# Optimization experiments

Measured on AMD Instinct MI355X. Metric: run time of the kernel, lower is better.

## Reference

```python
import jax, jax.numpy as jnp
import numpy as np

B, L, D, H = 64, 24, 512, 512


def setup_inputs() -> dict:
    key = jax.random.key(0)
    ks = jax.random.split(key, 6)
    inp = jax.random.normal(ks[0], (B, L, D), jnp.float32)
    length = jax.random.randint(ks[1], (B,), L // 2, L + 1)  # valid lengths in [L/2, L]
    # word_linear: word_dim -> 2*hidden_dim (kaiming normal, zero bias)
    word_W = jax.random.normal(ks[2], (2 * H, D), jnp.float32) * (2.0 / D) ** 0.5
    word_b = jnp.zeros((2 * H,), jnp.float32)
    # comp_linear: 2*hidden_dim -> 5*hidden_dim (TreeLSTM gates i, fl, fr, u, o)
    comp_W = jax.random.normal(ks[3], (5 * H, 2 * H), jnp.float32) * (1.0 / H) ** 0.5
    comp_b = jnp.zeros((5 * H,), jnp.float32)
    comp_query = jax.random.normal(ks[4], (H,), jnp.float32) * 0.01
    return dict(inp=inp, length=length, word_W=word_W, word_b=word_b,
                comp_W=comp_W, comp_b=comp_b, comp_query=comp_query)


def _tree_lstm_forward(inp, word_W, word_b, comp_W, comp_b, comp_query, length):
    max_depth = inp.shape[1]
    length_mask = jnp.arange(max_depth)[None, :] < length[:, None]  # (B, L) bool
    # leaf states: word_linear output chunked into (h, c)
    hc = inp @ word_W.T + word_b  # (B, L, 2H)
    h, c = jnp.split(hc, 2, axis=2)
    for i in range(max_depth - 1):  # sequential merge over shrinking length
        hl, cl = h[:, :-1, :], c[:, :-1, :]
        hr, cr = h[:, 1:, :], c[:, 1:, :]
        # BinaryTreeLSTMLayer: fused gate linear on [hl; hr]
        v = jnp.concatenate([hl, hr], axis=2) @ comp_W.T + comp_b  # (B, L-i-1, 5H)
        gi, gfl, gfr, gu, go = jnp.split(v, 5, axis=2)
        new_c = (cl * jax.nn.sigmoid(gfl + 1.0)
                 + cr * jax.nn.sigmoid(gfr + 1.0)
                 + jnp.tanh(gu) * jax.nn.sigmoid(gi))
        new_h = jax.nn.sigmoid(go) * jnp.tanh(new_c)
        if i < max_depth - 2:
            # select_composition: greedy (eval-mode) one-hot over query-dot scores
            scores = jnp.einsum('blh,h->bl', new_h, comp_query)  # (B, L-i-1)
            m = length_mask[:, i + 1:]
            masked = jnp.where(m, scores, -1e9)
            sel = jax.lax.stop_gradient(
                jax.nn.one_hot(jnp.argmax(masked, axis=1), masked.shape[1], dtype=new_h.dtype))
            cum = jnp.cumsum(sel, axis=1)
            left = 1.0 - cum
            right = jnp.concatenate(
                [jnp.zeros((sel.shape[0], 1), sel.dtype), cum[:, :-1]], axis=1)
            new_h = sel[..., None] * new_h + left[..., None] * hl + right[..., None] * hr
            new_c = sel[..., None] * new_c + left[..., None] * cl + right[..., None] * cr
        # update_state: only advance rows whose sequence is still active
        done = length_mask[:, i + 1].astype(new_h.dtype)[:, None, None]
        h = done * new_h + (1.0 - done) * h[:, :-1, :]
        c = done * new_c + (1.0 - done) * c[:, :-1, :]
    return h[:, 0, :]  # (B, H) root hidden state


def reference(inp, length, word_W, word_b, comp_W, comp_b, comp_query):
    return _tree_lstm_forward(inp, word_W, word_b, comp_W, comp_b, comp_query, length)
```

## Files before the change

### kernel.cpp

```cpp
#include <hip/hip_runtime.h>
#include <math.h>

#define BB 64
#define LL 24
#define DD 512
#define GG 2560
#define NSTEP 23
#define NTILES 160

__device__ __forceinline__ float sigm(float x) { return 1.0f / (1.0f + __expf(-x)); }

__device__ __forceinline__ unsigned short f2bf(float x) {
    unsigned u = __float_as_uint(x);
    unsigned r = (u + 0x7fff + ((u >> 16) & 1)) >> 16;
    return (unsigned short)r;
}
__device__ __forceinline__ float bf2f(unsigned short b) {
    return __uint_as_float(((unsigned)b) << 16);
}

using short8 = __attribute__((ext_vector_type(8))) short;
using f32x4 = __attribute__((ext_vector_type(4))) float;

__global__ __launch_bounds__(256) void splitW_k(const float* __restrict__ comp_W,
                                                unsigned short* __restrict__ Wh,
                                                unsigned short* __restrict__ Wl) {
    int t = (blockIdx.x * 256 + threadIdx.x) * 4;
    int n = t >> 9;
    int k = t & 511;
    const float* src = (n < GG) ? (comp_W + (size_t)n * (2 * DD) + k)
                                : (comp_W + (size_t)(n - GG) * (2 * DD) + DD + k);
    float4 v = *(const float4*)src;
    ushort4 h, l;
    h.x = f2bf(v.x); l.x = f2bf(v.x - bf2f(h.x));
    h.y = f2bf(v.y); l.y = f2bf(v.y - bf2f(h.y));
    h.z = f2bf(v.z); l.z = f2bf(v.z - bf2f(h.z));
    h.w = f2bf(v.w); l.w = f2bf(v.w - bf2f(h.w));
    *(ushort4*)(Wh + t) = h;
    *(ushort4*)(Wl + t) = l;
}

__global__ __launch_bounds__(256) void splitF_k(const float* __restrict__ src,
                                                unsigned short* __restrict__ dh,
                                                unsigned short* __restrict__ dl) {
    int t = (blockIdx.x * 256 + threadIdx.x) * 4;
    float4 v = *(const float4*)(src + t);
    ushort4 h, l;
    h.x = f2bf(v.x); l.x = f2bf(v.x - bf2f(h.x));
    h.y = f2bf(v.y); l.y = f2bf(v.y - bf2f(h.y));
    h.z = f2bf(v.z); l.z = f2bf(v.z - bf2f(h.z));
    h.w = f2bf(v.w); l.w = f2bf(v.w - bf2f(h.w));
    *(ushort4*)(dh + t) = h;
    *(ushort4*)(dl + t) = l;
}

__global__ __launch_bounds__(256) void gemm64w_mfma(
    const unsigned short* __restrict__ Ih, const unsigned short* __restrict__ Il,
    const unsigned short* __restrict__ Vh, const unsigned short* __restrict__ Vl,
    const float* __restrict__ bias,
    unsigned short* __restrict__ Ah, unsigned short* __restrict__ Al,
    float* __restrict__ O1) {
    __shared__ unsigned short AhS[64][72];
    __shared__ unsigned short AlS[64][72];
    __shared__ unsigned short BhS[128][72];
    __shared__ unsigned short BlS[128][72];

    const int tid = threadIdx.x;
    const int m0 = (blockIdx.x % 24) * 64;
    const int n0 = (blockIdx.x / 24) * 128;

    const int w = tid >> 6, lane = tid & 63;
    const int mq = w >> 1, nq = w & 1;
    const int lr = lane & 15, kg = lane >> 4;

    const int srow = tid >> 3;
    const int sk8 = tid & 7;

    const unsigned short* agh = Ih + (size_t)(m0 + srow) * DD + sk8 * 8;
    const unsigned short* agl = Il + (size_t)(m0 + srow) * DD + sk8 * 8;
    const unsigned short* bgh = Vh + (size_t)(n0 + srow) * DD + sk8 * 8;
    const unsigned short* bgl = Vl + (size_t)(n0 + srow) * DD + sk8 * 8;

    f32x4 acc[2][4];
#pragma unroll
    for (int mt = 0; mt < 2; ++mt)
#pragma unroll
        for (int nt = 0; nt < 4; ++nt) acc[mt][nt] = (f32x4){0.f, 0.f, 0.f, 0.f};

    short8 rAh[2], rAl[2], rBh[4], rBl[4];

#define LOADT(kt)                                                            \
    {                                                                        \
        _Pragma("unroll")                                                    \
        for (int it = 0; it < 2; ++it) {                                     \
            const size_t ro = (size_t)it * 32 * DD + (kt);                   \
            rAh[it] = *(const short8*)(agh + ro);                            \
            rAl[it] = *(const short8*)(agl + ro);                            \
        }                                                                    \
        _Pragma("unroll")                                                    \
        for (int it = 0; it < 4; ++it) {                                     \
            const size_t ro = (size_t)it * 32 * DD + (kt);                   \
            rBh[it] = *(const short8*)(bgh + ro);                            \
            rBl[it] = *(const short8*)(bgl + ro);                            \
        }                                                                    \
    }
#define WRITET()                                                             \
    {                                                                        \
        _Pragma("unroll")                                                    \
        for (int it = 0; it < 2; ++it) {                                     \
            const int row = srow + it * 32;                                  \
            *(short8*)&AhS[row][sk8 * 8] = rAh[it];                          \
            *(short8*)&AlS[row][sk8 * 8] = rAl[it];                          \
        }                                                                    \
        _Pragma("unroll")                                                    \
        for (int it = 0; it < 4; ++it) {                                     \
            const int row = srow + it * 32;                                  \
            *(short8*)&BhS[row][sk8 * 8] = rBh[it];                          \
            *(short8*)&BlS[row][sk8 * 8] = rBl[it];                          \
        }                                                                    \
    }

    LOADT(0);
    WRITET();
    __syncthreads();

    for (int kti = 0; kti < 8; ++kti) {
        if (kti + 1 < 8) LOADT((kti + 1) * 64);
#pragma unroll
        for (int ks2 = 0; ks2 < 2; ++ks2) {
            const int kb = ks2 * 32 + kg * 8;
            short8 fah[2], fal[2], fbh[4], fbl[4];
#pragma unroll
            for (int t = 0; t < 2; ++t) {
                fah[t] = *(const short8*)&AhS[mq * 32 + t * 16 + lr][kb];
                fal[t] = *(const short8*)&AlS[mq * 32 + t * 16 + lr][kb];
            }
#pragma unroll
            for (int t = 0; t < 4; ++t) {
                fbh[t] = *(const short8*)&BhS[nq * 64 + t * 16 + lr][kb];
                fbl[t] = *(const short8*)&BlS[nq * 64 + t * 16 + lr][kb];
            }
#pragma unroll
            for (int mt = 0; mt < 2; ++mt)
#pragma unroll
                for (int nt = 0; nt < 4; ++nt) {
                    acc[mt][nt] = __builtin_amdgcn_mfma_f32_16x16x32_bf16(fal[mt], fbh[nt], acc[mt][nt], 0, 0, 0);
                    acc[mt][nt] = __builtin_amdgcn_mfma_f32_16x16x32_bf16(fah[mt], fbl[nt], acc[mt][nt], 0, 0, 0);
                    acc[mt][nt] = __builtin_amdgcn_mfma_f32_16x16x32_bf16(fah[mt], fbh[nt], acc[mt][nt], 0, 0, 0);
                }
        }
        __syncthreads();
        if (kti + 1 < 8) {
            WRITET();
            __syncthreads();
        }
    }
#undef LOADT
#undef WRITET

#pragma unroll
    for (int mt = 0; mt < 2; ++mt) {
        const int mbase = m0 + mq * 32 + mt * 16 + kg * 4;
#pragma unroll
        for (int nt = 0; nt < 4; ++nt) {
            const int n = n0 + nq * 64 + nt * 16 + lr;
            const float bv = bias[n];
#pragma unroll
            for (int r = 0; r < 4; ++r) {
                const int m = mbase + r;
                float v = acc[mt][nt][r] + bv;
                if (n < DD) {
                    unsigned short hv = f2bf(v);
                    Ah[(size_t)m * DD + n] = hv;
                    Al[(size_t)m * DD + n] = f2bf(v - bf2f(hv));
                } else {
                    O1[(size_t)m * DD + (n - DD)] = v;
                }
            }
        }
    }
}

__global__ __launch_bounds__(256) void gemm_big_mfma(
    const unsigned short* __restrict__ Ah, const unsigned short* __restrict__ Al,
    const unsigned short* __restrict__ Wh, const unsigned short* __restrict__ Wl,
    float* __restrict__ O0, float* __restrict__ O1) {
    __shared__ unsigned short AhS[128][72];
    __shared__ unsigned short AlS[128][72];
    __shared__ unsigned short BhS[128][72];
    __shared__ unsigned short BlS[128][72];

    const int tid = threadIdx.x;
    const int xcd = blockIdx.x & 7, idx = blockIdx.x >> 3;
    const int n0 = (xcd * 5 + idx % 5) * 128;
    const int m0 = (idx / 5) * 128;

    const int w = tid >> 6, lane = tid & 63;
    const int mq = w >> 1, nq = w & 1;
    const int lr = lane & 15, kg = lane >> 4;

    const int srow = tid >> 3;
    const int sk8 = tid & 7;

    const unsigned short* agh = Ah + (size_t)(m0 + srow) * DD + sk8 * 8;
    const unsigned short* agl = Al + (size_t)(m0 + srow) * DD + sk8 * 8;
    const unsigned short* bgh = Wh + (size_t)(n0 + srow) * DD + sk8 * 8;
    const unsigned short* bgl = Wl + (size_t)(n0 + srow) * DD + sk8 * 8;

    f32x4 acc[4][4];
#pragma unroll
    for (int mt = 0; mt < 4; ++mt)
#pragma unroll
        for (int nt = 0; nt < 4; ++nt) acc[mt][nt] = (f32x4){0.f, 0.f, 0.f, 0.f};

    short8 rAh[4], rAl[4], rBh[4], rBl[4];

#define LOADT(kt)                                                            \
    {                                                                        \
        _Pragma("unroll")                                                    \
        for (int it = 0; it < 4; ++it) {                                     \
            const size_t ro = (size_t)it * 32 * DD + (kt);                   \
            rAh[it] = *(const short8*)(agh + ro);                            \
            rAl[it] = *(const short8*)(agl + ro);                            \
            rBh[it] = *(const short8*)(bgh + ro);                            \
            rBl[it] = *(const short8*)(bgl + ro);                            \
        }                                                                    \
    }
#define WRITET()                                                             \
    {                                                                        \
        _Pragma("unroll")                                                    \
        for (int it = 0; it < 4; ++it) {                                     \
            const int row = srow + it * 32;                                  \
            *(short8*)&AhS[row][sk8 * 8] = rAh[it];                          \
            *(short8*)&AlS[row][sk8 * 8] = rAl[it];                          \
            *(short8*)&BhS[row][sk8 * 8] = rBh[it];                          \
            *(short8*)&BlS[row][sk8 * 8] = rBl[it];                          \
        }                                                                    \
    }

    LOADT(0);
    WRITET();
    __syncthreads();

    for (int kti = 0; kti < 8; ++kti) {
        if (kti + 1 < 8) LOADT((kti + 1) * 64);
#pragma unroll
        for (int ks2 = 0; ks2 < 2; ++ks2) {
            const int kb = ks2 * 32 + kg * 8;
            short8 fah[4], fal[4], fbh[4], fbl[4];
#pragma unroll
            for (int t = 0; t < 4; ++t) {
                fah[t] = *(const short8*)&AhS[mq * 64 + t * 16 + lr][kb];
                fal[t] = *(const short8*)&AlS[mq * 64 + t * 16 + lr][kb];
                fbh[t] = *(const short8*)&BhS[nq * 64 + t * 16 + lr][kb];
                fbl[t] = *(const short8*)&BlS[nq * 64 + t * 16 + lr][kb];
            }
#pragma unroll
            for (int mt = 0; mt < 4; ++mt)
#pragma unroll
                for (int nt = 0; nt < 4; ++nt) {
                    acc[mt][nt] = __builtin_amdgcn_mfma_f32_16x16x32_bf16(fal[mt], fbh[nt], acc[mt][nt], 0, 0, 0);
                    acc[mt][nt] = __builtin_amdgcn_mfma_f32_16x16x32_bf16(fah[mt], fbl[nt], acc[mt][nt], 0, 0, 0);
                    acc[mt][nt] = __builtin_amdgcn_mfma_f32_16x16x32_bf16(fah[mt], fbh[nt], acc[mt][nt], 0, 0, 0);
                }
        }
        __syncthreads();
        if (kti + 1 < 8) {
            WRITET();
            __syncthreads();
        }
    }
#undef LOADT
#undef WRITET

#pragma unroll
    for (int mt = 0; mt < 4; ++mt) {
        const int mbase = m0 + mq * 64 + mt * 16 + kg * 4;
#pragma unroll
        for (int nt = 0; nt < 4; ++nt) {
            const int n = n0 + nq * 64 + nt * 16 + lr;
#pragma unroll
            for (int r = 0; r < 4; ++r) {
                const int m = mbase + r;
                float* dst = (n < GG) ? (O0 + (size_t)m * GG + n)
                                      : (O1 + (size_t)m * GG + (n - GG));
                *dst = acc[mt][nt][r];
            }
        }
    }
}

__device__ __forceinline__ float half_dot(const float* __restrict__ ar,
                                          const float* __restrict__ br,
                                          const float* __restrict__ cb,
                                          const float* __restrict__ cl,
                                          const float* __restrict__ cr,
                                          const float* __restrict__ q, int lane) {
    float part = 0.f;
#pragma unroll
    for (int d = lane; d < DD; d += 128) {
        float gi = ar[d] + br[d] + cb[d];
        float gfl = ar[DD + d] + br[DD + d] + cb[DD + d];
        float gfr = ar[2 * DD + d] + br[2 * DD + d] + cb[2 * DD + d];
        float gu = ar[3 * DD + d] + br[3 * DD + d] + cb[3 * DD + d];
        float go = ar[4 * DD + d] + br[4 * DD + d] + cb[4 * DD + d];
        float nc = cl[d] * sigm(gfl + 1.f) + cr[d] * sigm(gfr + 1.f) + tanhf(gu) * sigm(gi);
        part += sigm(go) * tanhf(nc) * q[d];
    }
#pragma unroll
    for (int off = 32; off; off >>= 1) part += __shfl_down(part, off);
    return part;
}

__device__ __forceinline__ void gate2n(const float* __restrict__ ar,
                                       const float* __restrict__ br,
                                       const float* __restrict__ cb,
                                       const float* __restrict__ cl,
                                       const float* __restrict__ cr, int d,
                                       float nh[2], float nc[2]) {
    float2 A0 = *(const float2*)(ar + d),          B0 = *(const float2*)(br + d);
    float2 A1 = *(const float2*)(ar + DD + d),     B1 = *(const float2*)(br + DD + d);
    float2 A2 = *(const float2*)(ar + 2 * DD + d), B2 = *(const float2*)(br + 2 * DD + d);
    float2 A3 = *(const float2*)(ar + 3 * DD + d), B3 = *(const float2*)(br + 3 * DD + d);
    float2 A4 = *(const float2*)(ar + 4 * DD + d), B4 = *(const float2*)(br + 4 * DD + d);
    float2 C0 = *(const float2*)(cb + d);
    float2 C1 = *(const float2*)(cb + DD + d);
    float2 C2 = *(const float2*)(cb + 2 * DD + d);
    float2 C3 = *(const float2*)(cb + 3 * DD + d);
    float2 C4 = *(const float2*)(cb + 4 * DD + d);
    float2 CL = *(const float2*)(cl + d);
    float2 CR = *(const float2*)(cr + d);
    float gi0 = A0.x + B0.x + C0.x, gi1 = A0.y + B0.y + C0.y;
    float gfl0 = A1.x + B1.x + C1.x, gfl1 = A1.y + B1.y + C1.y;
    float gfr0 = A2.x + B2.x + C2.x, gfr1 = A2.y + B2.y + C2.y;
    float gu0 = A3.x + B3.x + C3.x, gu1 = A3.y + B3.y + C3.y;
    float go0 = A4.x + B4.x + C4.x, go1 = A4.y + B4.y + C4.y;
    nc[0] = CL.x * sigm(gfl0 + 1.f) + CR.x * sigm(gfr0 + 1.f) + tanhf(gu0) * sigm(gi0);
    nc[1] = CL.y * sigm(gfl1 + 1.f) + CR.y * sigm(gfr1 + 1.f) + tanhf(gu1) * sigm(gi1);
    nh[0] = sigm(go0) * tanhf(nc[0]);
    nh[1] = sigm(go1) * tanhf(nc[1]);
}

__global__ __launch_bounds__(256) void scoreall_k(const float* __restrict__ acache,
                                                  const float* __restrict__ bcache,
                                                  const float* __restrict__ cbuf,
                                                  const float* __restrict__ compb,
                                                  const float* __restrict__ q,
                                                  float* __restrict__ scores_g) {
    __shared__ float red_s[4];
    const int tid = threadIdx.x;
    const int b = blockIdx.y;
    const int p = blockIdx.x * 2 + (tid >> 7);
    const bool valid = p < NSTEP;
    float w = 0.f;
    if (valid) {
        w = half_dot(acache + (size_t)(b * LL + p) * GG,
                     bcache + (size_t)(b * LL + p + 1) * GG, compb,
                     cbuf + (size_t)(b * LL + p) * DD,
                     cbuf + (size_t)(b * LL + p + 1) * DD, q, tid & 127);
    }
    if ((tid & 63) == 0) red_s[tid >> 6] = w;
    __syncthreads();
    if ((tid == 0 || tid == 128) && valid) {
        int base = tid >> 6;
        scores_g[b * NSTEP + p] = red_s[base] + red_s[base + 1];
    }
}

__global__ __launch_bounds__(256) void stepA_k(
    int i, const int* __restrict__ length, float* __restrict__ cbuf,
    const float* __restrict__ acache, const float* __restrict__ bcache,
    float* __restrict__ hout, unsigned short* __restrict__ hh,
    unsigned short* __restrict__ hl, float* __restrict__ scores_g,
    int* __restrict__ seq_g, int* __restrict__ kp_g, int* __restrict__ msel,
    const float* __restrict__ compb, const float* __restrict__ q, float* __restrict__ out) {
    __shared__ float red_s[4];
    __shared__ float sc_l[32];
    __shared__ int seq_l[32];
    __shared__ int k_sh;
    const int tid = threadIdx.x;
    const int b = blockIdx.x;
    const int lane7 = tid & 127;
    const int lenb = length[b];
    const int ncand = NSTEP - i;

    if (i == 0) {
        if (tid < LL) seq_l[tid] = tid;
    } else {
        if (tid < LL - i) seq_l[tid] = seq_g[b * 32 + tid];
    }
    if (tid < ncand) sc_l[tid] = scores_g[b * NSTEP + tid];
    __syncthreads();
    const int kp = (i > 0) ? kp_g[b] : 0;

    if (i > 0 && i < lenb) {
        int p = (tid < 128) ? (kp - 1) : kp;
        bool valid = (p >= 0) && (p < ncand);
        float w = 0.f;
        if (valid) {
            int sl = seq_l[p], sr = seq_l[p + 1];
            const float* ar = acache + (size_t)(b * LL + sl) * GG;
            const float* br = bcache + (size_t)(b * LL + sr) * GG;
            const float* cl = cbuf + (size_t)(b * LL + sl) * DD;
            const float* cr = cbuf + (size_t)(b * LL + sr) * DD;
#pragma unroll
            for (int pass = 0; pass < 2; ++pass) {
                int d = pass * 256 + lane7 * 2;
                float nh[2], nc[2];
                gate2n(ar, br, compb, cl, cr, d, nh, nc);
                float2 Q = *(const float2*)(q + d);
                w += nh[0] * Q.x + nh[1] * Q.y;
            }
#pragma unroll
            for (int off = 32; off; off >>= 1) w += __shfl_down(w, off);
        }
        if ((tid & 63) == 0) red_s[tid >> 6] = w;
        __syncthreads();
        if (tid == 0) {
            if (kp - 1 >= 0) sc_l[kp - 1] = red_s[0] + red_s[1];
            if (kp < ncand) sc_l[kp] = red_s[2] + red_s[3];
        }
        __syncthreads();
    }

    if (i + 1 < lenb) {
        if (tid == 0) {
            const int vmax = lenb - i - 2;
            int k = 0;
            float best = sc_l[0];
            for (int pp = 1; pp <= vmax; ++pp)
                if (sc_l[pp] > best) { best = sc_l[pp]; k = pp; }
            k_sh = k;
        }
        __syncthreads();
        const int k = k_sh;
        const int sl = seq_l[k], sr = seq_l[k + 1];
        const float* ar = acache + (size_t)(b * LL + sl) * GG;
        const float* br = bcache + (size_t)(b * LL + sr) * GG;
        const float* cl = cbuf + (size_t)(b * LL + sl) * DD;
        const float* cr = cbuf + (size_t)(b * LL + sr) * DD;
        {
            const int d = 2 * tid;
            float nh[2], nc[2];
            gate2n(ar, br, compb, cl, cr, d, nh, nc);
            *(float2*)(cbuf + (size_t)(b * LL + sl) * DD + d) = make_float2(nc[0], nc[1]);
            *(float2*)(hout + (size_t)b * DD + d) = make_float2(nh[0], nh[1]);
            ushort2 hv, lv;
            hv.x = f2bf(nh[0]); lv.x = f2bf(nh[0] - bf2f(hv.x));
            hv.y = f2bf(nh[1]); lv.y = f2bf(nh[1] - bf2f(hv.y));
            *(ushort2*)(hh + (size_t)b * DD + d) = hv;
            *(ushort2*)(hl + (size_t)b * DD + d) = lv;
            if (i == NSTEP - 1)
                *(float2*)(out + (size_t)b * DD + d) = make_float2(nh[0], nh[1]);
        }
        float sv = (tid + 1 < ncand) ? sc_l[tid + 1] : 0.f;
        int qv = (tid + 1 < LL - i) ? seq_l[tid + 1] : 0;
        __syncthreads();
        if (tid >= k + 1 && tid <= ncand - 2) sc_l[tid] = sv;
        if (tid >= k + 1 && tid <= LL - i - 2) seq_l[tid] = qv;
        if (tid < ncand - 1) scores_g[b * NSTEP + tid] = sc_l[tid];
        if (tid < LL - i - 1) seq_g[b * 32 + tid] = seq_l[tid];
        if (tid == 0) { kp_g[b] = k; msel[b] = sl; }
    } else if (i == NSTEP - 1) {
        const int d = 2 * tid;
        *(float2*)(out + (size_t)b * DD + d) = *(const float2*)(hout + (size_t)b * DD + d);
    }
}

__global__ __launch_bounds__(256) void stepB_mfma(
    const unsigned short* __restrict__ hh, const unsigned short* __restrict__ hl,
    const int* __restrict__ msel,
    const unsigned short* __restrict__ Wh, const unsigned short* __restrict__ Wl,
    float* __restrict__ acache, float* __restrict__ bcache) {
    __shared__ int msel_s[BB];
    const int tid = threadIdx.x;
    const int bid = blockIdx.x;
    if (tid < BB) msel_s[tid] = msel[tid];
    __syncthreads();

    const int w = tid >> 6, lane = tid & 63;
    const int mt0 = (w >> 1) * 2;
    const int nt = w & 1;
    const int lr = lane & 15;
    const int kg = lane >> 4;
    const int n = bid * 32 + nt * 16 + lr;

    const unsigned short* wh_row = Wh + (size_t)n * DD;
    const unsigned short* wl_row = Wl + (size_t)n * DD;
    const unsigned short* a0h_row = hh + (size_t)(mt0 * 16 + lr) * DD;
    const unsigned short* a0l_row = hl + (size_t)(mt0 * 16 + lr) * DD;
    const unsigned short* a1h_row = a0h_row + 16 * DD;
    const unsigned short* a1l_row = a0l_row + 16 * DD;

    f32x4 acc0 = {0.f, 0.f, 0.f, 0.f};
    f32x4 acc1 = {0.f, 0.f, 0.f, 0.f};

#pragma unroll 4
    for (int ks = 0; ks < 16; ++ks) {
        const int kb = ks * 32 + kg * 8;
        short8 bh = *(const short8*)(wh_row + kb);
        short8 bl = *(const short8*)(wl_row + kb);
        short8 a0h = *(const short8*)(a0h_row + kb);
        short8 a0l = *(const short8*)(a0l_row + kb);
        short8 a1h = *(const short8*)(a1h_row + kb);
        short8 a1l = *(const short8*)(a1l_row + kb);
        acc0 = __builtin_amdgcn_mfma_f32_16x16x32_bf16(a0h, bh, acc0, 0, 0, 0);
        acc1 = __builtin_amdgcn_mfma_f32_16x16x32_bf16(a1h, bh, acc1, 0, 0, 0);
        acc0 = __builtin_amdgcn_mfma_f32_16x16x32_bf16(a0l, bh, acc0, 0, 0, 0);
        acc1 = __builtin_amdgcn_mfma_f32_16x16x32_bf16(a1l, bh, acc1, 0, 0, 0);
        acc0 = __builtin_amdgcn_mfma_f32_16x16x32_bf16(a0h, bl, acc0, 0, 0, 0);
        acc1 = __builtin_amdgcn_mfma_f32_16x16x32_bf16(a1h, bl, acc1, 0, 0, 0);
    }

#pragma unroll
    for (int t = 0; t < 2; ++t) {
        f32x4 acc = t ? acc1 : acc0;
        const int mbase = (mt0 + t) * 16 + kg * 4;
#pragma unroll
        for (int r = 0; r < 4; ++r) {
            int m = mbase + r;
            size_t row = (size_t)(m * LL + msel_s[m]);
            float* dst = (n < GG) ? (acache + row * GG + n)
                                  : (bcache + row * GG + (n - GG));
            *dst = acc[r];
        }
    }
}

extern "C" void kernel_launch(void* const* d_in, const int* in_sizes, int n_in, void* d_out,
                              int out_size, void* d_ws, size_t ws_size, hipStream_t stream) {
    const float* inp = (const float*)d_in[0];
    const int* length = (const int*)d_in[1];
    const float* word_W = (const float*)d_in[2];
    const float* word_b = (const float*)d_in[3];
    const float* comp_W = (const float*)d_in[4];
    const float* comp_b = (const float*)d_in[5];
    const float* comp_q = (const float*)d_in[6];
    float* out = (float*)d_out;

    float* ws = (float*)d_ws;
    size_t off = 0;
    float* cbuf = ws + off;   off += (size_t)BB * LL * DD;
    float* acache = ws + off; off += (size_t)BB * LL * GG;
    float* bcache = ws + off; off += (size_t)BB * LL * GG;
    float* hout = ws + off;   off += (size_t)BB * DD;
    float* scores = ws + off; off += 2048;
    int* seq_g = (int*)(ws + off); off += BB * 32;
    int* kp_g = (int*)(ws + off);  off += 64;
    int* msel = (int*)(ws + off);  off += 64;
    unsigned short* Wh = (unsigned short*)(ws + off); off += (size_t)5120 * DD / 2;
    unsigned short* Wl = (unsigned short*)(ws + off); off += (size_t)5120 * DD / 2;
    unsigned short* hh = (unsigned short*)(ws + off); off += (size_t)BB * DD / 2;
    unsigned short* hl = (unsigned short*)(ws + off); off += (size_t)BB * DD / 2;
    unsigned short* Ah = (unsigned short*)(ws + off); off += (size_t)BB * LL * DD / 2;
    unsigned short* Al = (unsigned short*)(ws + off); off += (size_t)BB * LL * DD / 2;
    unsigned short* Ih = (unsigned short*)(ws + off); off += (size_t)BB * LL * DD / 2;
    unsigned short* Il = (unsigned short*)(ws + off); off += (size_t)BB * LL * DD / 2;
    unsigned short* Vh = (unsigned short*)(ws + off); off += (size_t)1024 * DD / 2;
    unsigned short* Vl = (unsigned short*)(ws + off); off += (size_t)1024 * DD / 2;
    (void)ws_size; (void)in_sizes; (void)n_in; (void)out_size;

    splitW_k<<<2560, 256, 0, stream>>>(comp_W, Wh, Wl);
    splitF_k<<<768, 256, 0, stream>>>(inp, Ih, Il);
    splitF_k<<<512, 256, 0, stream>>>(word_W, Vh, Vl);

    gemm64w_mfma<<<192, 256, 0, stream>>>(Ih, Il, Vh, Vl, word_b, Ah, Al, cbuf);

    gemm_big_mfma<<<480, 256, 0, stream>>>(Ah, Al, Wh, Wl, acache, bcache);

    scoreall_k<<<dim3(12, 64), 256, 0, stream>>>(acache, bcache, cbuf, comp_b, comp_q, scores);

    for (int i = 0; i < NSTEP; ++i) {
        stepA_k<<<BB, 256, 0, stream>>>(i, length, cbuf, acache, bcache, hout, hh, hl,
                                        scores, seq_g, kp_g, msel, comp_b, comp_q, out);
        if (i < NSTEP - 1) {
            stepB_mfma<<<NTILES, 256, 0, stream>>>(hh, hl, msel, Wh, Wl, acache, bcache);
        }
    }
}
```

Measured before the change: 585.2 us.

## Interleave gate columns and fuse neighbor rescoring into stepB GEMM epilogue

The comp_W rows and bias are permuted so the five gates for each pair of hidden units sit next to each other, letting each stepB block own complete gate groups. The re-scoring of the two candidates next to the merged node moves out of the serial stepA kernel and into the stepB epilogue. There it runs on freshly computed gate values kept in shared memory and is accumulated into scores with atomics, while stepA zeroes those slots beforehand. This shortens the latency-bound per-step stepA work at the cost of more complex stepB tiles (128 blocks with padded 48-wide N tiles) and atomic accumulation order.

```diff
diff --git a/kernel.cpp b/kernel.cpp
--- a/kernel.cpp
+++ b/kernel.cpp
@@ -6,7 +6,8 @@
 #define DD 512
 #define GG 2560
 #define NSTEP 23
-#define NTILES 160
+#define NBB 128
+
 
 __device__ __forceinline__ float sigm(float x) { return 1.0f / (1.0f + __expf(-x)); }
 
@@ -21,6 +22,26 @@
 
 using short8 = __attribute__((ext_vector_type(8))) short;
 using f32x4 = __attribute__((ext_vector_type(4))) float;
+
+__device__ __forceinline__ void gatepair(const float* ar, const float* br,
+                                         const float* cb,
+                                         float cl0, float cl1, float cr0, float cr1,
+                                         float nh[2], float nc[2]) {
+    float2 A0 = *(const float2*)(ar + 0), B0 = *(const float2*)(br + 0), C0 = *(const float2*)(cb + 0);
+    float2 A1 = *(const float2*)(ar + 2), B1 = *(const float2*)(br + 2), C1 = *(const float2*)(cb + 2);
+    float2 A2 = *(const float2*)(ar + 4), B2 = *(const float2*)(br + 4), C2 = *(const float2*)(cb + 4);
+    float2 A3 = *(const float2*)(ar + 6), B3 = *(const float2*)(br + 6), C3 = *(const float2*)(cb + 6);
+    float2 A4 = *(const float2*)(ar + 8), B4 = *(const float2*)(br + 8), C4 = *(const float2*)(cb + 8);
+    float gi0 = A0.x + B0.x + C0.x, gi1 = A0.y + B0.y + C0.y;
+    float gfl0 = A1.x + B1.x + C1.x, gfl1 = A1.y + B1.y + C1.y;
+    float gfr0 = A2.x + B2.x + C2.x, gfr1 = A2.y + B2.y + C2.y;
+    float gu0 = A3.x + B3.x + C3.x, gu1 = A3.y + B3.y + C3.y;
+    float go0 = A4.x + B4.x + C4.x, go1 = A4.y + B4.y + C4.y;
+    nc[0] = cl0 * sigm(gfl0 + 1.f) + cr0 * sigm(gfr0 + 1.f) + tanhf(gu0) * sigm(gi0);
+    nc[1] = cl1 * sigm(gfl1 + 1.f) + cr1 * sigm(gfr1 + 1.f) + tanhf(gu1) * sigm(gi1);
+    nh[0] = sigm(go0) * tanhf(nc[0]);
+    nh[1] = sigm(go1) * tanhf(nc[1]);
+}
 
 __global__ __launch_bounds__(256) void splitW_k(const float* __restrict__ comp_W,
                                                 unsigned short* __restrict__ Wh,
@@ -28,8 +49,11 @@
     int t = (blockIdx.x * 256 + threadIdx.x) * 4;
     int n = t >> 9;
     int k = t & 511;
-    const float* src = (n < GG) ? (comp_W + (size_t)n * (2 * DD) + k)
-                                : (comp_W + (size_t)(n - GG) * (2 * DD) + DD + k);
+    int p = (n >= GG) ? 1 : 0;
+    int r = n - p * GG;
+    int g = (r % 10) >> 1;
+    int d = (r / 10) * 2 + (r & 1);
+    const float* src = comp_W + (size_t)(g * 512 + d) * (2 * DD) + p * DD + k;
     float4 v = *(const float4*)src;
     ushort4 h, l;
     h.x = f2bf(v.x); l.x = f2bf(v.x - bf2f(h.x));
@@ -38,6 +62,14 @@
     h.w = f2bf(v.w); l.w = f2bf(v.w - bf2f(h.w));
     *(ushort4*)(Wh + t) = h;
     *(ushort4*)(Wl + t) = l;
+}
+
+__global__ __launch_bounds__(256) void compbp_k(const float* __restrict__ comp_b,
+                                                float* __restrict__ cbp) {
+    int c = blockIdx.x * 256 + threadIdx.x;
+    int g = (c % 10) >> 1;
+    int d = (c / 10) * 2 + (c & 1);
+    cbp[c] = comp_b[g * 512 + d];
 }
 
 __global__ __launch_bounds__(256) void splitF_k(const float* __restrict__ src,
@@ -292,59 +324,29 @@
 
 __device__ __forceinline__ float half_dot(const float* __restrict__ ar,
                                           const float* __restrict__ br,
-                                          const float* __restrict__ cb,
+                                          const float* __restrict__ cbp,
                                           const float* __restrict__ cl,
                                           const float* __restrict__ cr,
                                           const float* __restrict__ q, int lane) {
     float part = 0.f;
 #pragma unroll
-    for (int d = lane; d < DD; d += 128) {
-        float gi = ar[d] + br[d] + cb[d];
-        float gfl = ar[DD + d] + br[DD + d] + cb[DD + d];
-        float gfr = ar[2 * DD + d] + br[2 * DD + d] + cb[2 * DD + d];
-        float gu = ar[3 * DD + d] + br[3 * DD + d] + cb[3 * DD + d];
-        float go = ar[4 * DD + d] + br[4 * DD + d] + cb[4 * DD + d];
-        float nc = cl[d] * sigm(gfl + 1.f) + cr[d] * sigm(gfr + 1.f) + tanhf(gu) * sigm(gi);
-        part += sigm(go) * tanhf(nc) * q[d];
+    for (int pr = lane; pr < 256; pr += 128) {
+        const int base = pr * 10, d0 = pr * 2;
+        float nh[2], nc[2];
+        gatepair(ar + base, br + base, cbp + base,
+                 cl[d0], cl[d0 + 1], cr[d0], cr[d0 + 1], nh, nc);
+        float2 Q = *(const float2*)(q + d0);
+        part += nh[0] * Q.x + nh[1] * Q.y;
     }
 #pragma unroll
     for (int off = 32; off; off >>= 1) part += __shfl_down(part, off);
     return part;
-}
-
-__device__ __forceinline__ void gate2n(const float* __restrict__ ar,
-                                       const float* __restrict__ br,
-                                       const float* __restrict__ cb,
-                                       const float* __restrict__ cl,
-                                       const float* __restrict__ cr, int d,
-                                       float nh[2], float nc[2]) {
-    float2 A0 = *(const float2*)(ar + d),          B0 = *(const float2*)(br + d);
-    float2 A1 = *(const float2*)(ar + DD + d),     B1 = *(const float2*)(br + DD + d);
-    float2 A2 = *(const float2*)(ar + 2 * DD + d), B2 = *(const float2*)(br + 2 * DD + d);
-    float2 A3 = *(const float2*)(ar + 3 * DD + d), B3 = *(const float2*)(br + 3 * DD + d);
-    float2 A4 = *(const float2*)(ar + 4 * DD + d), B4 = *(const float2*)(br + 4 * DD + d);
-    float2 C0 = *(const float2*)(cb + d);
-    float2 C1 = *(const float2*)(cb + DD + d);
-    float2 C2 = *(const float2*)(cb + 2 * DD + d);
-    float2 C3 = *(const float2*)(cb + 3 * DD + d);
-    float2 C4 = *(const float2*)(cb + 4 * DD + d);
-    float2 CL = *(const float2*)(cl + d);
-    float2 CR = *(const float2*)(cr + d);
-    float gi0 = A0.x + B0.x + C0.x, gi1 = A0.y + B0.y + C0.y;
-    float gfl0 = A1.x + B1.x + C1.x, gfl1 = A1.y + B1.y + C1.y;
-    float gfr0 = A2.x + B2.x + C2.x, gfr1 = A2.y + B2.y + C2.y;
-    float gu0 = A3.x + B3.x + C3.x, gu1 = A3.y + B3.y + C3.y;
-    float go0 = A4.x + B4.x + C4.x, go1 = A4.y + B4.y + C4.y;
-    nc[0] = CL.x * sigm(gfl0 + 1.f) + CR.x * sigm(gfr0 + 1.f) + tanhf(gu0) * sigm(gi0);
-    nc[1] = CL.y * sigm(gfl1 + 1.f) + CR.y * sigm(gfr1 + 1.f) + tanhf(gu1) * sigm(gi1);
-    nh[0] = sigm(go0) * tanhf(nc[0]);
-    nh[1] = sigm(go1) * tanhf(nc[1]);
 }
 
 __global__ __launch_bounds__(256) void scoreall_k(const float* __restrict__ acache,
                                                   const float* __restrict__ bcache,
                                                   const float* __restrict__ cbuf,
-                                                  const float* __restrict__ compb,
+                                                  const float* __restrict__ cbp,
                                                   const float* __restrict__ q,
                                                   float* __restrict__ scores_g) {
     __shared__ float red_s[4];
@@ -355,7 +357,7 @@
     float w = 0.f;
     if (valid) {
         w = half_dot(acache + (size_t)(b * LL + p) * GG,
-                     bcache + (size_t)(b * LL + p + 1) * GG, compb,
+                     bcache + (size_t)(b * LL + p + 1) * GG, cbp,
                      cbuf + (size_t)(b * LL + p) * DD,
                      cbuf + (size_t)(b * LL + p + 1) * DD, q, tid & 127);
     }
@@ -372,15 +374,14 @@
     const float* __restrict__ acache, const float* __restrict__ bcache,
     float* __restrict__ hout, unsigned short* __restrict__ hh,
     unsigned short* __restrict__ hl, float* __restrict__ scores_g,
-    int* __restrict__ seq_g, int* __restrict__ kp_g, int* __restrict__ msel,
-    const float* __restrict__ compb, const float* __restrict__ q, float* __restrict__ out) {
-    __shared__ float red_s[4];
+    int* __restrict__ seq_g, int4* __restrict__ rescInfo, int* __restrict__ msel,
+    const float* __restrict__ cbp, const float* __restrict__ q,
+    float* __restrict__ out) {
     __shared__ float sc_l[32];
     __shared__ int seq_l[32];
     __shared__ int k_sh;
     const int tid = threadIdx.x;
     const int b = blockIdx.x;
-    const int lane7 = tid & 127;
     const int lenb = length[b];
     const int ncand = NSTEP - i;
 
@@ -391,37 +392,6 @@
     }
     if (tid < ncand) sc_l[tid] = scores_g[b * NSTEP + tid];
     __syncthreads();
-    const int kp = (i > 0) ? kp_g[b] : 0;
-
-    if (i > 0 && i < lenb) {
-        int p = (tid < 128) ? (kp - 1) : kp;
-        bool valid = (p >= 0) && (p < ncand);
-        float w = 0.f;
-        if (valid) {
-            int sl = seq_l[p], sr = seq_l[p + 1];
-            const float* ar = acache + (size_t)(b * LL + sl) * GG;
-            const float* br = bcache + (size_t)(b * LL + sr) * GG;
-            const float* cl = cbuf + (size_t)(b * LL + sl) * DD;
-            const float* cr = cbuf + (size_t)(b * LL + sr) * DD;
-#pragma unroll
-            for (int pass = 0; pass < 2; ++pass) {
-                int d = pass * 256 + lane7 * 2;
-                float nh[2], nc[2];
-                gate2n(ar, br, compb, cl, cr, d, nh, nc);
-                float2 Q = *(const float2*)(q + d);
-                w += nh[0] * Q.x + nh[1] * Q.y;
-            }
-#pragma unroll
-            for (int off = 32; off; off >>= 1) w += __shfl_down(w, off);
-        }
-        if ((tid & 63) == 0) red_s[tid >> 6] = w;
-        __syncthreads();
-        if (tid == 0) {
-            if (kp - 1 >= 0) sc_l[kp - 1] = red_s[0] + red_s[1];
-            if (kp < ncand) sc_l[kp] = red_s[2] + red_s[3];
-        }
-        __syncthreads();
-    }
 
     if (i + 1 < lenb) {
         if (tid == 0) {
@@ -435,14 +405,20 @@
         __syncthreads();
         const int k = k_sh;
         const int sl = seq_l[k], sr = seq_l[k + 1];
+        int sLn = 0, sRn = 0;
+        if (tid == 0) {
+            sLn = (k > 0) ? seq_l[k - 1] : 0;
+            sRn = (k < ncand - 1) ? seq_l[k + 2] : 0;
+        }
         const float* ar = acache + (size_t)(b * LL + sl) * GG;
         const float* br = bcache + (size_t)(b * LL + sr) * GG;
         const float* cl = cbuf + (size_t)(b * LL + sl) * DD;
         const float* cr = cbuf + (size_t)(b * LL + sr) * DD;
         {
-            const int d = 2 * tid;
+            const int d = 2 * tid, base = tid * 10;
             float nh[2], nc[2];
-            gate2n(ar, br, compb, cl, cr, d, nh, nc);
+            gatepair(ar + base, br + base, cbp + base,
+                     cl[d], cl[d + 1], cr[d], cr[d + 1], nh, nc);
             *(float2*)(cbuf + (size_t)(b * LL + sl) * DD + d) = make_float2(nc[0], nc[1]);
             *(float2*)(hout + (size_t)b * DD + d) = make_float2(nh[0], nh[1]);
             ushort2 hv, lv;
@@ -458,71 +434,130 @@
         __syncthreads();
         if (tid >= k + 1 && tid <= ncand - 2) sc_l[tid] = sv;
         if (tid >= k + 1 && tid <= LL - i - 2) seq_l[tid] = qv;
-        if (tid < ncand - 1) scores_g[b * NSTEP + tid] = sc_l[tid];
+        if (tid < ncand - 1)
+            scores_g[b * NSTEP + tid] = (tid == k - 1 || tid == k) ? 0.f : sc_l[tid];
         if (tid < LL - i - 1) seq_g[b * 32 + tid] = seq_l[tid];
-        if (tid == 0) { kp_g[b] = k; msel[b] = sl; }
-    } else if (i == NSTEP - 1) {
-        const int d = 2 * tid;
-        *(float2*)(out + (size_t)b * DD + d) = *(const float2*)(hout + (size_t)b * DD + d);
+        if (tid == 0) {
+            msel[b] = sl;
+            int fl = ((k > 0) ? 1 : 0) | ((k < ncand - 1) ? 2 : 0);
+            rescInfo[b] = make_int4(k, sLn, sRn, fl);
+        }
+    } else {
+        if (tid == 0) rescInfo[b] = make_int4(0, 0, 0, 0);
+        if (i == NSTEP - 1) {
+            const int d = 2 * tid;
+            *(float2*)(out + (size_t)b * DD + d) = *(const float2*)(hout + (size_t)b * DD + d);
+        }
     }
 }
 
 __global__ __launch_bounds__(256) void stepB_mfma(
     const unsigned short* __restrict__ hh, const unsigned short* __restrict__ hl,
-    const int* __restrict__ msel,
+    const int* __restrict__ msel, const int4* __restrict__ rescInfo,
     const unsigned short* __restrict__ Wh, const unsigned short* __restrict__ Wl,
-    float* __restrict__ acache, float* __restrict__ bcache) {
+    const float* __restrict__ cbuf, const float* __restrict__ cbp,
+    const float* __restrict__ q,
+    float* __restrict__ acache, float* __restrict__ bcache,
+    float* __restrict__ scores_g) {
+    __shared__ float newv[64][44];
     __shared__ int msel_s[BB];
+    __shared__ int4 ri_s[BB];
     const int tid = threadIdx.x;
-    const int bid = blockIdx.x;
-    if (tid < BB) msel_s[tid] = msel[tid];
+    const int j = blockIdx.x;
+    if (tid < BB) { msel_s[tid] = msel[tid]; ri_s[tid] = rescInfo[tid]; }
     __syncthreads();
 
     const int w = tid >> 6, lane = tid & 63;
-    const int mt0 = (w >> 1) * 2;
-    const int nt = w & 1;
-    const int lr = lane & 15;
-    const int kg = lane >> 4;
-    const int n = bid * 32 + nt * 16 + lr;
-
-    const unsigned short* wh_row = Wh + (size_t)n * DD;
-    const unsigned short* wl_row = Wl + (size_t)n * DD;
-    const unsigned short* a0h_row = hh + (size_t)(mt0 * 16 + lr) * DD;
-    const unsigned short* a0l_row = hl + (size_t)(mt0 * 16 + lr) * DD;
-    const unsigned short* a1h_row = a0h_row + 16 * DD;
-    const unsigned short* a1l_row = a0l_row + 16 * DD;
+    const int lr = lane & 15, kg = lane >> 4;
+
+    int wr[3];
+#pragma unroll
+    for (int nt = 0; nt < 3; ++nt) {
+        int t = nt * 16 + lr;
+        wr[nt] = (t < 20) ? (j * 20 + t) : ((t < 40) ? (GG + j * 20 + (t - 20)) : 0);
+    }
+    const unsigned short* b0h = Wh + (size_t)wr[0] * DD;
+    const unsigned short* b0l = Wl + (size_t)wr[0] * DD;
+    const unsigned short* b1h = Wh + (size_t)wr[1] * DD;
+    const unsigned short* b1l = Wl + (size_t)wr[1] * DD;
+    const unsigned short* b2h = Wh + (size_t)wr[2] * DD;
+    const unsigned short* b2l = Wl + (size_t)wr[2] * DD;
+    const unsigned short* arow_h = hh + (size_t)(w * 16 + lr) * DD;
+    const unsigned short* arow_l = hl + (size_t)(w * 16 + lr) * DD;
 
     f32x4 acc0 = {0.f, 0.f, 0.f, 0.f};
     f32x4 acc1 = {0.f, 0.f, 0.f, 0.f};
+    f32x4 acc2 = {0.f, 0.f, 0.f, 0.f};
 
 #pragma unroll 4
     for (int ks = 0; ks < 16; ++ks) {
         const int kb = ks * 32 + kg * 8;
-        short8 bh = *(const short8*)(wh_row + kb);
-        short8 bl = *(const short8*)(wl_row + kb);
-        short8 a0h = *(const short8*)(a0h_row + kb);
-        short8 a0l = *(const short8*)(a0l_row + kb);
-        short8 a1h = *(const short8*)(a1h_row + kb);
-        short8 a1l = *(const short8*)(a1l_row + kb);
-        acc0 = __builtin_amdgcn_mfma_f32_16x16x32_bf16(a0h, bh, acc0, 0, 0, 0);
-        acc1 = __builtin_amdgcn_mfma_f32_16x16x32_bf16(a1h, bh, acc1, 0, 0, 0);
-        acc0 = __builtin_amdgcn_mfma_f32_16x16x32_bf16(a0l, bh, acc0, 0, 0, 0);
-        acc1 = __builtin_amdgcn_mfma_f32_16x16x32_bf16(a1l, bh, acc1, 0, 0, 0);
-        acc0 = __builtin_amdgcn_mfma_f32_16x16x32_bf16(a0h, bl, acc0, 0, 0, 0);
-        acc1 = __builtin_amdgcn_mfma_f32_16x16x32_bf16(a1h, bl, acc1, 0, 0, 0);
-    }
-
-#pragma unroll
-    for (int t = 0; t < 2; ++t) {
-        f32x4 acc = t ? acc1 : acc0;
-        const int mbase = (mt0 + t) * 16 + kg * 4;
-#pragma unroll
-        for (int r = 0; r < 4; ++r) {
-            int m = mbase + r;
-            size_t row = (size_t)(m * LL + msel_s[m]);
-            float* dst = (n < GG) ? (acache + row * GG + n)
-                                  : (bcache + row * GG + (n - GG));
-            *dst = acc[r];
+        short8 ah = *(const short8*)(arow_h + kb);
+        short8 al = *(const short8*)(arow_l + kb);
+        short8 w0h = *(const short8*)(b0h + kb), w0l = *(const short8*)(b0l + kb);
+        short8 w1h = *(const short8*)(b1h + kb), w1l = *(const short8*)(b1l + kb);
+        short8 w2h = *(const short8*)(b2h + kb), w2l = *(const short8*)(b2l + kb);
+        acc0 = __builtin_amdgcn_mfma_f32_16x16x32_bf16(al, w0h, acc0, 0, 0, 0);
+        acc1 = __builtin_amdgcn_mfma_f32_16x16x32_bf16(al, w1h, acc1, 0, 0, 0);
+        acc2 = __builtin_amdgcn_mfma_f32_16x16x32_bf16(al, w2h, acc2, 0, 0, 0);
+        acc0 = __builtin_amdgcn_mfma_f32_16x16x32_bf16(ah, w0l, acc0, 0, 0, 0);
+        acc1 = __builtin_amdgcn_mfma_f32_16x16x32_bf16(ah, w1l, acc1, 0, 0, 0);
+        acc2 = __builtin_amdgcn_mfma_f32_16x16x32_bf16(ah, w2l, acc2, 0, 0, 0);
+        acc0 = __builtin_amdgcn_mfma_f32_16x16x32_bf16(ah, w0h, acc0, 0, 0, 0);
+        acc1 = __builtin_amdgcn_mfma_f32_16x16x32_bf16(ah, w1h, acc1, 0, 0, 0);
+        acc2 = __builtin_amdgcn_mfma_f32_16x16x32_bf16(ah, w2h, acc2, 0, 0, 0);
+    }
+
+#pragma unroll
+    for (int nt = 0; nt < 3; ++nt) {
+        f32x4 a = (nt == 0) ? acc0 : (nt == 1) ? acc1 : acc2;
+        const int t = nt * 16 + lr;
+        if (t < 40) {
+#pragma unroll
+            for (int r = 0; r < 4; ++r) {
+                const int bb = w * 16 + kg * 4 + r;
+                newv[bb][t] = a[r];
+                size_t row = (size_t)(bb * LL + msel_s[bb]);
+                float* dst = (t < 20) ? (acache + row * GG + j * 20 + t)
+                                      : (bcache + row * GG + j * 20 + (t - 20));
+                *dst = a[r];
+            }
+        }
+    }
+    __syncthreads();
+
+    if (tid < 128) {
+        const int bb = tid >> 1, pp = tid & 1;
+        const int4 ri = ri_s[bb];
+        const int k = ri.x, sL = ri.y, sR = ri.z, fl = ri.w;
+        const int sN = msel_s[bb];
+        const int gbase = j * 20 + pp * 10;
+        const int d0 = (2 * j + pp) * 2;
+        float2 Q = *(const float2*)(q + d0);
+        float s0 = 0.f, s1 = 0.f;
+        if (fl & 1) {
+            const float* arow = acache + (size_t)(bb * LL + sL) * GG + gbase;
+            const float* clp = cbuf + (size_t)(bb * LL + sL) * DD;
+            const float* crp = cbuf + (size_t)(bb * LL + sN) * DD;
+            float nh[2], nc[2];
+            gatepair(arow, &newv[bb][20 + pp * 10], cbp + gbase,
+                     clp[d0], clp[d0 + 1], crp[d0], crp[d0 + 1], nh, nc);
+            s0 = nh[0] * Q.x + nh[1] * Q.y;
+        }
+        if (fl & 2) {
+            const float* brow = bcache + (size_t)(bb * LL + sR) * GG + gbase;
+            const float* clp = cbuf + (size_t)(bb * LL + sN) * DD;
+            const float* crp = cbuf + (size_t)(bb * LL + sR) * DD;
+            float nh[2], nc[2];
+            gatepair(&newv[bb][pp * 10], brow, cbp + gbase,
+                     clp[d0], clp[d0 + 1], crp[d0], crp[d0 + 1], nh, nc);
+            s1 = nh[0] * Q.x + nh[1] * Q.y;
+        }
+        s0 += __shfl_xor(s0, 1);
+        s1 += __shfl_xor(s1, 1);
+        if (pp == 0) {
+            if (fl & 1) atomicAdd(scores_g + bb * NSTEP + (k - 1), s0);
+            if (fl & 2) atomicAdd(scores_g + bb * NSTEP + k, s1);
         }
     }
 }
@@ -546,8 +581,9 @@
     float* hout = ws + off;   off += (size_t)BB * DD;
     float* scores = ws + off; off += 2048;
     int* seq_g = (int*)(ws + off); off += BB * 32;
-    int* kp_g = (int*)(ws + off);  off += 64;
+    int4* rescInfo = (int4*)(ws + off); off += BB * 4;
     int* msel = (int*)(ws + off);  off += 64;
+    float* cbp = ws + off;    off += GG;
     unsigned short* Wh = (unsigned short*)(ws + off); off += (size_t)5120 * DD / 2;
     unsigned short* Wl = (unsigned short*)(ws + off); off += (size_t)5120 * DD / 2;
     unsigned short* hh = (unsigned short*)(ws + off); off += (size_t)BB * DD / 2;
@@ -561,6 +597,7 @@
     (void)ws_size; (void)in_sizes; (void)n_in; (void)out_size;
 
     splitW_k<<<2560, 256, 0, stream>>>(comp_W, Wh, Wl);
+    compbp_k<<<10, 256, 0, stream>>>(comp_b, cbp);
     splitF_k<<<768, 256, 0, stream>>>(inp, Ih, Il);
     splitF_k<<<512, 256, 0, stream>>>(word_W, Vh, Vl);
 
@@ -568,13 +605,15 @@
 
     gemm_big_mfma<<<480, 256, 0, stream>>>(Ah, Al, Wh, Wl, acache, bcache);
 
-    scoreall_k<<<dim3(12, 64), 256, 0, stream>>>(acache, bcache, cbuf, comp_b, comp_q, scores);
+    scoreall_k<<<dim3(12, 64), 256, 0, stream>>>(acache, bcache, cbuf, cbp, comp_q, scores);
 
     for (int i = 0; i < NSTEP; ++i) {
         stepA_k<<<BB, 256, 0, stream>>>(i, length, cbuf, acache, bcache, hout, hh, hl,
-                                        scores, seq_g, kp_g, msel, comp_b, comp_q, out);
+                                        scores, seq_g, rescInfo, msel, cbp, comp_q, out);
         if (i < NSTEP - 1) {
-            stepB_mfma<<<NTILES, 256, 0, stream>>>(hh, hl, msel, Wh, Wl, acache, bcache);
-        }
-    }
-}
+            stepB_mfma<<<NBB, 256, 0, stream>>>(hh, hl, msel, rescInfo, Wh, Wl,
+                                                cbuf, cbp, comp_q,
+                                                acache, bcache, scores);
+        }
+    }
+}
```

Result: slower. 721.5 us (+23.3%).

## Interleave gate rows of comp_W so each thread reads contiguous gate pairs

Applied to the files above, without the earlier changes.

The comp_W rows, and with them the acache/bcache gate columns and the bias, are permuted so that the five gates for each pair of hidden units sit in ten contiguous floats. The gate elementwise code then reads one contiguous 40-byte block per pair instead of five strided float2 loads spread 2KB apart. A small kernel builds the permuted bias. The cost is per-thread accesses that are less coalesced across lanes, since the lane stride becomes 40 bytes.

```diff
diff --git a/kernel.cpp b/kernel.cpp
--- a/kernel.cpp
+++ b/kernel.cpp
@@ -8,6 +8,7 @@
 #define NSTEP 23
 #define NTILES 160
 
+
 __device__ __forceinline__ float sigm(float x) { return 1.0f / (1.0f + __expf(-x)); }
 
 __device__ __forceinline__ unsigned short f2bf(float x) {
@@ -21,6 +22,26 @@
 
 using short8 = __attribute__((ext_vector_type(8))) short;
 using f32x4 = __attribute__((ext_vector_type(4))) float;
+
+__device__ __forceinline__ void gatepair(const float* ar, const float* br,
+                                         const float* cb,
+                                         float cl0, float cl1, float cr0, float cr1,
+                                         float nh[2], float nc[2]) {
+    float2 A0 = *(const float2*)(ar + 0), B0 = *(const float2*)(br + 0), C0 = *(const float2*)(cb + 0);
+    float2 A1 = *(const float2*)(ar + 2), B1 = *(const float2*)(br + 2), C1 = *(const float2*)(cb + 2);
+    float2 A2 = *(const float2*)(ar + 4), B2 = *(const float2*)(br + 4), C2 = *(const float2*)(cb + 4);
+    float2 A3 = *(const float2*)(ar + 6), B3 = *(const float2*)(br + 6), C3 = *(const float2*)(cb + 6);
+    float2 A4 = *(const float2*)(ar + 8), B4 = *(const float2*)(br + 8), C4 = *(const float2*)(cb + 8);
+    float gi0 = A0.x + B0.x + C0.x, gi1 = A0.y + B0.y + C0.y;
+    float gfl0 = A1.x + B1.x + C1.x, gfl1 = A1.y + B1.y + C1.y;
+    float gfr0 = A2.x + B2.x + C2.x, gfr1 = A2.y + B2.y + C2.y;
+    float gu0 = A3.x + B3.x + C3.x, gu1 = A3.y + B3.y + C3.y;
+    float go0 = A4.x + B4.x + C4.x, go1 = A4.y + B4.y + C4.y;
+    nc[0] = cl0 * sigm(gfl0 + 1.f) + cr0 * sigm(gfr0 + 1.f) + tanhf(gu0) * sigm(gi0);
+    nc[1] = cl1 * sigm(gfl1 + 1.f) + cr1 * sigm(gfr1 + 1.f) + tanhf(gu1) * sigm(gi1);
+    nh[0] = sigm(go0) * tanhf(nc[0]);
+    nh[1] = sigm(go1) * tanhf(nc[1]);
+}
 
 __global__ __launch_bounds__(256) void splitW_k(const float* __restrict__ comp_W,
                                                 unsigned short* __restrict__ Wh,
@@ -28,8 +49,11 @@
     int t = (blockIdx.x * 256 + threadIdx.x) * 4;
     int n = t >> 9;
     int k = t & 511;
-    const float* src = (n < GG) ? (comp_W + (size_t)n * (2 * DD) + k)
-                                : (comp_W + (size_t)(n - GG) * (2 * DD) + DD + k);
+    int p = (n >= GG) ? 1 : 0;
+    int r = n - p * GG;
+    int g = (r % 10) >> 1;
+    int d = (r / 10) * 2 + (r & 1);
+    const float* src = comp_W + (size_t)(g * 512 + d) * (2 * DD) + p * DD + k;
     float4 v = *(const float4*)src;
     ushort4 h, l;
     h.x = f2bf(v.x); l.x = f2bf(v.x - bf2f(h.x));
@@ -38,6 +62,14 @@
     h.w = f2bf(v.w); l.w = f2bf(v.w - bf2f(h.w));
     *(ushort4*)(Wh + t) = h;
     *(ushort4*)(Wl + t) = l;
+}
+
+__global__ __launch_bounds__(256) void compbp_k(const float* __restrict__ comp_b,
+                                                float* __restrict__ cbp) {
+    int c = blockIdx.x * 256 + threadIdx.x;
+    int g = (c % 10) >> 1;
+    int d = (c / 10) * 2 + (c & 1);
+    cbp[c] = comp_b[g * 512 + d];
 }
 
 __global__ __launch_bounds__(256) void splitF_k(const float* __restrict__ src,
@@ -292,59 +324,29 @@
 
 __device__ __forceinline__ float half_dot(const float* __restrict__ ar,
                                           const float* __restrict__ br,
-                                          const float* __restrict__ cb,
+                                          const float* __restrict__ cbp,
                                           const float* __restrict__ cl,
                                           const float* __restrict__ cr,
                                           const float* __restrict__ q, int lane) {
     float part = 0.f;
 #pragma unroll
-    for (int d = lane; d < DD; d += 128) {
-        float gi = ar[d] + br[d] + cb[d];
-        float gfl = ar[DD + d] + br[DD + d] + cb[DD + d];
-        float gfr = ar[2 * DD + d] + br[2 * DD + d] + cb[2 * DD + d];
-        float gu = ar[3 * DD + d] + br[3 * DD + d] + cb[3 * DD + d];
-        float go = ar[4 * DD + d] + br[4 * DD + d] + cb[4 * DD + d];
-        float nc = cl[d] * sigm(gfl + 1.f) + cr[d] * sigm(gfr + 1.f) + tanhf(gu) * sigm(gi);
-        part += sigm(go) * tanhf(nc) * q[d];
+    for (int pr = lane; pr < 256; pr += 128) {
+        const int base = pr * 10, d0 = pr * 2;
+        float nh[2], nc[2];
+        gatepair(ar + base, br + base, cbp + base,
+                 cl[d0], cl[d0 + 1], cr[d0], cr[d0 + 1], nh, nc);
+        float2 Q = *(const float2*)(q + d0);
+        part += nh[0] * Q.x + nh[1] * Q.y;
     }
 #pragma unroll
     for (int off = 32; off; off >>= 1) part += __shfl_down(part, off);
     return part;
-}
-
-__device__ __forceinline__ void gate2n(const float* __restrict__ ar,
-                                       const float* __restrict__ br,
-                                       const float* __restrict__ cb,
-                                       const float* __restrict__ cl,
-                                       const float* __restrict__ cr, int d,
-                                       float nh[2], float nc[2]) {
-    float2 A0 = *(const float2*)(ar + d),          B0 = *(const float2*)(br + d);
-    float2 A1 = *(const float2*)(ar + DD + d),     B1 = *(const float2*)(br + DD + d);
-    float2 A2 = *(const float2*)(ar + 2 * DD + d), B2 = *(const float2*)(br + 2 * DD + d);
-    float2 A3 = *(const float2*)(ar + 3 * DD + d), B3 = *(const float2*)(br + 3 * DD + d);
-    float2 A4 = *(const float2*)(ar + 4 * DD + d), B4 = *(const float2*)(br + 4 * DD + d);
-    float2 C0 = *(const float2*)(cb + d);
-    float2 C1 = *(const float2*)(cb + DD + d);
-    float2 C2 = *(const float2*)(cb + 2 * DD + d);
-    float2 C3 = *(const float2*)(cb + 3 * DD + d);
-    float2 C4 = *(const float2*)(cb + 4 * DD + d);
-    float2 CL = *(const float2*)(cl + d);
-    float2 CR = *(const float2*)(cr + d);
-    float gi0 = A0.x + B0.x + C0.x, gi1 = A0.y + B0.y + C0.y;
-    float gfl0 = A1.x + B1.x + C1.x, gfl1 = A1.y + B1.y + C1.y;
-    float gfr0 = A2.x + B2.x + C2.x, gfr1 = A2.y + B2.y + C2.y;
-    float gu0 = A3.x + B3.x + C3.x, gu1 = A3.y + B3.y + C3.y;
-    float go0 = A4.x + B4.x + C4.x, go1 = A4.y + B4.y + C4.y;
-    nc[0] = CL.x * sigm(gfl0 + 1.f) + CR.x * sigm(gfr0 + 1.f) + tanhf(gu0) * sigm(gi0);
-    nc[1] = CL.y * sigm(gfl1 + 1.f) + CR.y * sigm(gfr1 + 1.f) + tanhf(gu1) * sigm(gi1);
-    nh[0] = sigm(go0) * tanhf(nc[0]);
-    nh[1] = sigm(go1) * tanhf(nc[1]);
 }
 
 __global__ __launch_bounds__(256) void scoreall_k(const float* __restrict__ acache,
                                                   const float* __restrict__ bcache,
                                                   const float* __restrict__ cbuf,
-                                                  const float* __restrict__ compb,
+                                                  const float* __restrict__ cbp,
                                                   const float* __restrict__ q,
                                                   float* __restrict__ scores_g) {
     __shared__ float red_s[4];
@@ -355,7 +357,7 @@
     float w = 0.f;
     if (valid) {
         w = half_dot(acache + (size_t)(b * LL + p) * GG,
-                     bcache + (size_t)(b * LL + p + 1) * GG, compb,
+                     bcache + (size_t)(b * LL + p + 1) * GG, cbp,
                      cbuf + (size_t)(b * LL + p) * DD,
                      cbuf + (size_t)(b * LL + p + 1) * DD, q, tid & 127);
     }
@@ -373,14 +375,14 @@
     float* __restrict__ hout, unsigned short* __restrict__ hh,
     unsigned short* __restrict__ hl, float* __restrict__ scores_g,
     int* __restrict__ seq_g, int* __restrict__ kp_g, int* __restrict__ msel,
-    const float* __restrict__ compb, const float* __restrict__ q, float* __restrict__ out) {
+    const float* __restrict__ cbp, const float* __restrict__ q,
+    float* __restrict__ out) {
     __shared__ float red_s[4];
     __shared__ float sc_l[32];
     __shared__ int seq_l[32];
     __shared__ int k_sh;
     const int tid = threadIdx.x;
     const int b = blockIdx.x;
-    const int lane7 = tid & 127;
     const int lenb = length[b];
     const int ncand = NSTEP - i;
 
@@ -399,20 +401,10 @@
         float w = 0.f;
         if (valid) {
             int sl = seq_l[p], sr = seq_l[p + 1];
-            const float* ar = acache + (size_t)(b * LL + sl) * GG;
-            const float* br = bcache + (size_t)(b * LL + sr) * GG;
-            const float* cl = cbuf + (size_t)(b * LL + sl) * DD;
-            const float* cr = cbuf + (size_t)(b * LL + sr) * DD;
-#pragma unroll
-            for (int pass = 0; pass < 2; ++pass) {
-                int d = pass * 256 + lane7 * 2;
-                float nh[2], nc[2];
-                gate2n(ar, br, compb, cl, cr, d, nh, nc);
-                float2 Q = *(const float2*)(q + d);
-                w += nh[0] * Q.x + nh[1] * Q.y;
-            }
-#pragma unroll
-            for (int off = 32; off; off >>= 1) w += __shfl_down(w, off);
+            w = half_dot(acache + (size_t)(b * LL + sl) * GG,
+                         bcache + (size_t)(b * LL + sr) * GG, cbp,
+                         cbuf + (size_t)(b * LL + sl) * DD,
+                         cbuf + (size_t)(b * LL + sr) * DD, q, tid & 127);
         }
         if ((tid & 63) == 0) red_s[tid >> 6] = w;
         __syncthreads();
@@ -440,9 +432,10 @@
         const float* cl = cbuf + (size_t)(b * LL + sl) * DD;
         const float* cr = cbuf + (size_t)(b * LL + sr) * DD;
         {
-            const int d = 2 * tid;
+            const int d = 2 * tid, base = tid * 10;
             float nh[2], nc[2];
-            gate2n(ar, br, compb, cl, cr, d, nh, nc);
+            gatepair(ar + base, br + base, cbp + base,
+                     cl[d], cl[d + 1], cr[d], cr[d + 1], nh, nc);
             *(float2*)(cbuf + (size_t)(b * LL + sl) * DD + d) = make_float2(nc[0], nc[1]);
             *(float2*)(hout + (size_t)b * DD + d) = make_float2(nh[0], nh[1]);
             ushort2 hv, lv;
@@ -548,6 +541,7 @@
     int* seq_g = (int*)(ws + off); off += BB * 32;
     int* kp_g = (int*)(ws + off);  off += 64;
     int* msel = (int*)(ws + off);  off += 64;
+    float* cbp = ws + off;    off += GG;
     unsigned short* Wh = (unsigned short*)(ws + off); off += (size_t)5120 * DD / 2;
     unsigned short* Wl = (unsigned short*)(ws + off); off += (size_t)5120 * DD / 2;
     unsigned short* hh = (unsigned short*)(ws + off); off += (size_t)BB * DD / 2;
@@ -561,6 +555,7 @@
     (void)ws_size; (void)in_sizes; (void)n_in; (void)out_size;
 
     splitW_k<<<2560, 256, 0, stream>>>(comp_W, Wh, Wl);
+    compbp_k<<<10, 256, 0, stream>>>(comp_b, cbp);
     splitF_k<<<768, 256, 0, stream>>>(inp, Ih, Il);
     splitF_k<<<512, 256, 0, stream>>>(word_W, Vh, Vl);
 
@@ -568,11 +563,11 @@
 
     gemm_big_mfma<<<480, 256, 0, stream>>>(Ah, Al, Wh, Wl, acache, bcache);
 
-    scoreall_k<<<dim3(12, 64), 256, 0, stream>>>(acache, bcache, cbuf, comp_b, comp_q, scores);
+    scoreall_k<<<dim3(12, 64), 256, 0, stream>>>(acache, bcache, cbuf, cbp, comp_q, scores);
 
     for (int i = 0; i < NSTEP; ++i) {
         stepA_k<<<BB, 256, 0, stream>>>(i, length, cbuf, acache, bcache, hout, hh, hl,
-                                        scores, seq_g, kp_g, msel, comp_b, comp_q, out);
+                                        scores, seq_g, kp_g, msel, cbp, comp_q, out);
         if (i < NSTEP - 1) {
             stepB_mfma<<<NTILES, 256, 0, stream>>>(hh, hl, msel, Wh, Wl, acache, bcache);
         }
```

Result: no change. 587.9 us (+0.4%).
